# Kernel optimization log

Hardware: AMD Instinct MI355X
Metric: run time of the kernel (lower is better)

Reference implementation:

```python
import jax, jax.numpy as jnp
import numpy as np

H = 4            # num_heads
D_HID = 128      # n_hidden (per head)
IN = 256         # in_feats
C = 47           # n_classes
NEG = 0.2        # DGL GATConv default negative_slope
NUM_SRC = (150000, 25000, 6000)
NUM_DST = (25000, 6000, 1024)
NUM_EDGES = (375000, 90000, 10240)


def gat_conv(h_src, h_dst, src, dst, Wsrc, Wdst, al, ar, b, num_dst, out_dim, apply_act):
    # h_src: [Ns, Fin], h_dst: [Nd, Fin]; Wsrc/Wdst: [H*out, Fin]; al/ar: [H, out]; b: [H*out]
    fs = (h_src @ Wsrc.T).reshape(-1, H, out_dim)          # [Ns,H,out]
    fd = (h_dst @ Wdst.T).reshape(-1, H, out_dim)          # [Nd,H,out]
    el = jnp.einsum('nhd,hd->nh', fs, al)                  # [Ns,H]
    er = jnp.einsum('nhd,hd->nh', fd, ar)                  # [Nd,H]
    e = jax.nn.leaky_relu(el[src] + er[dst], NEG)          # [E,H]
    # numerically-stable edge softmax per dst node
    m = jax.ops.segment_max(e, dst, num_segments=num_dst)  # [Nd,H]
    m = jnp.where(jnp.isfinite(m), m, 0.0)                 # guard isolated dst nodes
    ex = jnp.exp(e - m[dst])                               # [E,H]
    s = jax.ops.segment_sum(ex, dst, num_segments=num_dst) # [Nd,H]
    # weighted neighbor aggregation (scatter-add), normalize after the sum
    agg = jax.ops.segment_sum(ex[:, :, None] * fs[src], dst, num_segments=num_dst)  # [Nd,H,out]
    rst = agg / jnp.maximum(s, 1e-9)[:, :, None]
    rst = rst + b.reshape(1, H, out_dim)
    if apply_act:
        rst = jax.nn.elu(rst)
    return rst


def setup_inputs() -> dict:
    key = jax.random.key(0)
    ks = jax.random.split(key, 32)
    inp = {}
    inp['x'] = jax.random.normal(ks[0], (NUM_SRC[0], IN), dtype=jnp.float32)
    # sampled blocks as edge lists (dst nodes are prefix of src nodes)
    inp['src0'] = jax.random.randint(ks[1], (NUM_EDGES[0],), 0, NUM_SRC[0])
    inp['dst0'] = jax.random.randint(ks[2], (NUM_EDGES[0],), 0, NUM_DST[0])
    inp['src1'] = jax.random.randint(ks[3], (NUM_EDGES[1],), 0, NUM_SRC[1])
    inp['dst1'] = jax.random.randint(ks[4], (NUM_EDGES[1],), 0, NUM_DST[1])
    inp['src2'] = jax.random.randint(ks[5], (NUM_EDGES[2],), 0, NUM_SRC[2])
    inp['dst2'] = jax.random.randint(ks[6], (NUM_EDGES[2],), 0, NUM_DST[2])
    # layer params: (in_dim, out_per_head): (256,128), (512,128), (512,47)
    dims = [(IN, D_HID), (H * D_HID, D_HID), (H * D_HID, C)]
    k = 7
    for l, (fin, fout) in enumerate(dims):
        inp[f'Wsrc{l}'] = jax.random.normal(ks[k], (H * fout, fin), dtype=jnp.float32) * 0.05; k += 1
        inp[f'Wdst{l}'] = jax.random.normal(ks[k], (H * fout, fin), dtype=jnp.float32) * 0.05; k += 1
        inp[f'al{l}'] = jax.random.normal(ks[k], (H, fout), dtype=jnp.float32) * 0.05; k += 1
        inp[f'ar{l}'] = jax.random.normal(ks[k], (H, fout), dtype=jnp.float32) * 0.05; k += 1
        inp[f'b{l}'] = jnp.zeros((H * fout,), dtype=jnp.float32); k += 1
    return inp


def reference(x, src0, dst0, src1, dst1, src2, dst2,
              Wsrc0, Wdst0, al0, ar0, b0,
              Wsrc1, Wdst1, al1, ar1, b1,
              Wsrc2, Wdst2, al2, ar2, b2):
    h = x
    # layer 0
    h = gat_conv(h, h[:NUM_DST[0]], src0, dst0, Wsrc0, Wdst0, al0, ar0, b0,
                 NUM_DST[0], D_HID, True).reshape(NUM_DST[0], H * D_HID)
    # layer 1
    h = gat_conv(h, h[:NUM_DST[1]], src1, dst1, Wsrc1, Wdst1, al1, ar1, b1,
                 NUM_DST[1], D_HID, True).reshape(NUM_DST[1], H * D_HID)
    # layer 2 (no activation), mean over heads, log-softmax
    h = gat_conv(h, h[:NUM_DST[2]], src2, dst2, Wsrc2, Wdst2, al2, ar2, b2,
                 NUM_DST[2], C, False)                      # [1024,H,C]
    h = h.mean(axis=1)                                      # [1024,C]
    return jax.nn.log_softmax(h, axis=-1)
```

## Files before the change

### kernel.cpp

```cpp
#include <hip/hip_runtime.h>
#include <math.h>


#define E0 375000
#define E1 90000
#define E2 10240
#define ETOT (E0 + E1 + E2)
#define ND0 25000
#define ND1 6000
#define ND2 1024
#define NTOT (ND0 + ND1 + ND2)
#define NCH ((NTOT + 127) / 128)

static const int L_NS[3]   = {150000, 25000, 6000};
static const int L_ND[3]   = {ND0, ND1, ND2};
static const int L_FIN[3]  = {256, 512, 512};
static const int L_FOUT[3] = {128, 128, 47};

typedef short bf8_t __attribute__((ext_vector_type(8)));
typedef float f32x4 __attribute__((ext_vector_type(4)));

__device__ __forceinline__ float lrelu(float v) { return v >= 0.f ? v : 0.2f * v; }
__device__ __forceinline__ unsigned short f2b(float f) {
  unsigned u = __float_as_uint(f);
  unsigned r = u + 0x7fffu + ((u >> 16) & 1u);
  return (unsigned short)(r >> 16);
}
__device__ __forceinline__ float b2f(unsigned v) {
  return __uint_as_float(v << 16);
}

__device__ __forceinline__ void gload16(const unsigned short* g, unsigned short* l) {
  __builtin_amdgcn_global_load_lds(
      (const __attribute__((address_space(1))) unsigned int*)g,
      (__attribute__((address_space(3))) unsigned int*)l, 16, 0, 0);
}


__global__ void k_prep_count(
    const int* __restrict__ d0, const int* __restrict__ d1,
    const int* __restrict__ d2, int* __restrict__ cntAll, int* __restrict__ r,
    const float* __restrict__ Ws0, const float* __restrict__ Wd0,
    const float* __restrict__ al0, const float* __restrict__ ar0,
    const float* __restrict__ Ws1, const float* __restrict__ Wd1,
    const float* __restrict__ al1, const float* __restrict__ ar1,
    const float* __restrict__ Ws2, const float* __restrict__ Wd2,
    const float* __restrict__ al2, const float* __restrict__ ar2,
    unsigned short* __restrict__ wlrb, float* __restrict__ wlr1,
    float* __restrict__ wlr2,
    unsigned short* __restrict__ B0, unsigned short* __restrict__ B1,
    unsigned short* __restrict__ B2) {
  int gid = blockIdx.x * 256 + threadIdx.x;
  if (gid < ETOT) {
    int goff, dv;
    if (gid < E0) { goff = 0; dv = d0[gid]; }
    else if (gid < E0 + E1) { goff = ND0; dv = d1[gid - E0]; }
    else { goff = ND0 + ND1; dv = d2[gid - E0 - E1]; }
    r[gid] = atomicAdd(&cntAll[goff + dv], 1);
  }
  if (gid < 2048) {
    int h = gid >> 8, k = gid & 255;
    const float* W = (h < 4) ? Ws0 : Wd0;
    const float* a = (h < 4) ? al0 : ar0;
    int hh = h & 3;
    float acc = 0.f;
    for (int d = 0; d < 128; ++d)
      acc += a[hh * 128 + d] * W[(size_t)(hh * 128 + d) * 256 + k];
    wlrb[h * 264 + k] = f2b(acc);
  } else if (gid < 4096) {
    int idx = gid - 2048;
    wlrb[(8 + (idx >> 8)) * 264 + (idx & 255)] = 0;
  } else if (gid < 12288) {
    int idx = gid - 4096;
    float* wlr; const float *Ws, *Wd, *al, *ar; int Fout;
    if (idx < 4096) { wlr = wlr1; Ws = Ws1; Wd = Wd1; al = al1; ar = ar1; Fout = 128; }
    else { idx -= 4096; wlr = wlr2; Ws = Ws2; Wd = Wd2; al = al2; ar = ar2; Fout = 47; }
    int which = idx >> 11;
    int rem = idx & 2047;
    int h = rem >> 9, k = rem & 511;
    const float* W = which ? Wd : Ws;
    const float* a = which ? ar : al;
    float acc = 0.f;
    for (int d = 0; d < Fout; ++d)
      acc += a[h * Fout + d] * W[(size_t)(h * Fout + d) * 512 + k];
    wlr[which * 2048 + rem] = acc;
  }
  const int n0 = 512 * 256, n1 = 512 * 512, n2 = 188 * 512;
  for (int i = gid; i < n0 + n1 + n2; i += gridDim.x * 256) {
    if (i < n0) B0[i] = f2b(Ws0[i]);
    else if (i < n0 + n1) B1[i - n0] = f2b(Ws1[i - n0]);
    else B2[i - n0 - n1] = f2b(Ws2[i - n0 - n1]);
  }
}

__global__ __launch_bounds__(128) void k_scanA(const int* __restrict__ cnt,
                                               int* __restrict__ S,
                                               int* __restrict__ btot, int n) {
  __shared__ int wt[2];
  int c = blockIdx.x, t = threadIdx.x, lane = t & 63, w = t >> 6;
  int g = c * 128 + t;
  int v = (g < n) ? cnt[g] : 0;
  int incl = v;
  for (int off = 1; off < 64; off <<= 1) {
    int u = __shfl_up(incl, off);
    if (lane >= off) incl += u;
  }
  if (lane == 63) wt[w] = incl;
  __syncthreads();
  int base = (w == 1) ? wt[0] : 0;
  if (g < n) S[g] = incl - v + base;
  if (t == 127) btot[c] = wt[0] + wt[1];
}

__global__ __launch_bounds__(256) void k_scanB(const int* __restrict__ btot,
                                               int* __restrict__ S, int n, int etot) {
  __shared__ int tv[256];
  int c = blockIdx.x, t = threadIdx.x;
  int own = (t < NCH) ? btot[t] : 0;
  tv[t] = own;
  __syncthreads();
  for (int off = 1; off < 256; off <<= 1) {
    int u = (t >= off) ? tv[t - off] : 0;
    __syncthreads();
    tv[t] += u;
    __syncthreads();
  }
  int base = tv[c] - btot[c];
  int g = c * 128 + (t & 127);
  if (t < 128 && g < n) S[g] += base;
  if (c == 0 && t == 255) S[n] = etot;
}

__global__ void k_scatter_all(
    const int* __restrict__ s0, const int* __restrict__ d0,
    const int* __restrict__ s1, const int* __restrict__ d1,
    const int* __restrict__ s2, const int* __restrict__ d2,
    const int* __restrict__ S, const int* __restrict__ r,
    int* __restrict__ cvAll) {
  int g = blockIdx.x * 256 + threadIdx.x;
  if (g >= ETOT) return;
  int goff, dv, sv;
  if (g < E0) { goff = 0; dv = d0[g]; sv = s0[g]; }
  else if (g < E0 + E1) { int e = g - E0; goff = ND0; dv = d1[e]; sv = s1[e]; }
  else { int e = g - E0 - E1; goff = ND0 + ND1; dv = d2[e]; sv = s2[e]; }
  cvAll[S[goff + dv] + r[g]] = sv;
}


__global__ __launch_bounds__(256) void k_dotc_mfma(
    const float* __restrict__ x, const unsigned short* __restrict__ wlrb,
    float* __restrict__ ell, float* __restrict__ err, int Ns, int Nd) {
  __shared__ unsigned short As[128 * 72];
  __shared__ unsigned short Bs[16 * 264];
  const int tid = threadIdx.x;
  const int w = tid >> 6, lane = tid & 63;
  const int bm = blockIdx.x * 128;
  const int rowg = tid >> 4;
  const int seg  = tid & 15;
  for (int i = tid; i < 16 * 264; i += 256) Bs[i] = wlrb[i];
  f32x4 acc[2] = {};
  for (int k0 = 0; k0 < 256; k0 += 64) {
    __syncthreads();
#pragma unroll
    for (int i = 0; i < 8; ++i) {
      int row = rowg + i * 16;
      int gm = bm + row;
      int gmc = gm < Ns ? gm : Ns - 1;
      float4 a = *reinterpret_cast<const float4*>(x + (size_t)gmc * 256 + k0 + seg * 4);
      ushort4 ub;
      ub.x = f2b(a.x); ub.y = f2b(a.y); ub.z = f2b(a.z); ub.w = f2b(a.w);
      *reinterpret_cast<ushort4*>(&As[row * 72 + seg * 4]) = ub;
    }
    __syncthreads();
    const int ra = w * 32 + (lane & 15);
    const int kf = (lane >> 4) * 8;
#pragma unroll
    for (int ks = 0; ks < 2; ++ks) {
      bf8_t b0 = *reinterpret_cast<const bf8_t*>(&Bs[(lane & 15) * 264 + k0 + ks * 32 + kf]);
      bf8_t a0 = *reinterpret_cast<const bf8_t*>(&As[ra * 72 + ks * 32 + kf]);
      bf8_t a1 = *reinterpret_cast<const bf8_t*>(&As[(ra + 16) * 72 + ks * 32 + kf]);
      acc[0] = __builtin_amdgcn_mfma_f32_16x16x32_bf16(a0, b0, acc[0], 0, 0, 0);
      acc[1] = __builtin_amdgcn_mfma_f32_16x16x32_bf16(a1, b0, acc[1], 0, 0, 0);
    }
  }
  int col = lane & 15;
#pragma unroll
  for (int fm = 0; fm < 2; ++fm) {
#pragma unroll
    for (int j = 0; j < 4; ++j) {
      int node = bm + w * 32 + fm * 16 + (lane >> 4) * 4 + j;
      if (node >= Ns) continue;
      float v = acc[fm][j];
      if (col < 4) ell[(size_t)node * 4 + col] = v;
      else if (col < 8 && node < Nd) err[(size_t)node * 4 + (col - 4)] = v;
    }
  }
}

__device__ __forceinline__ void reduce8_store(float v[8], int lane, int node, int Nd,
                                              float* __restrict__ ell,
                                              float* __restrict__ err) {
#pragma unroll
  for (int h = 0; h < 8; ++h) {
    v[h] += __shfl_xor(v[h], 8);
    v[h] += __shfl_xor(v[h], 16);
    v[h] += __shfl_xor(v[h], 32);
  }
  int sel = lane >> 3;
  float t01 = (sel & 1) ? v[1] : v[0];
  float t23 = (sel & 1) ? v[3] : v[2];
  float t45 = (sel & 1) ? v[5] : v[4];
  float t67 = (sel & 1) ? v[7] : v[6];
  float t03 = (sel & 2) ? t23 : t01;
  float t47 = (sel & 2) ? t67 : t45;
  float s   = (sel & 4) ? t47 : t03;
  s += __shfl_xor(s, 1);
  s += __shfl_xor(s, 2);
  s += __shfl_xor(s, 4);
  if ((lane & 7) == 0) {
    if (sel < 4) ell[(size_t)node * 4 + sel] = s;
    else if (node < Nd) err[(size_t)node * 4 + (sel - 4)] = s;
  }
}

__global__ __launch_bounds__(256) void k_dot_bf(
    const unsigned short* __restrict__ Hs, const float* __restrict__ wlr,
    float* __restrict__ ell, float* __restrict__ err, int Ns, int Nd) {
  int node = blockIdx.x * 4 + (threadIdx.x >> 6);
  int lane = threadIdx.x & 63;
  if (node >= Ns) return;
  uint4 raw = *reinterpret_cast<const uint4*>(Hs + (size_t)node * 512 + lane * 8);
  float xv[8];
  xv[0] = b2f(raw.x & 0xffffu); xv[1] = b2f(raw.x >> 16);
  xv[2] = b2f(raw.y & 0xffffu); xv[3] = b2f(raw.y >> 16);
  xv[4] = b2f(raw.z & 0xffffu); xv[5] = b2f(raw.z >> 16);
  xv[6] = b2f(raw.w & 0xffffu); xv[7] = b2f(raw.w >> 16);
  bool nR = node < Nd;
  float v[8];
#pragma unroll
  for (int h = 0; h < 4; ++h) {
    const float* wp = wlr + h * 512 + lane * 8;
    float4 w0 = *reinterpret_cast<const float4*>(wp);
    float4 w1 = *reinterpret_cast<const float4*>(wp + 4);
    v[h] = xv[0]*w0.x + xv[1]*w0.y + xv[2]*w0.z + xv[3]*w0.w +
           xv[4]*w1.x + xv[5]*w1.y + xv[6]*w1.z + xv[7]*w1.w;
    v[4 + h] = 0.f;
    if (nR) {
      const float* wq = wlr + 2048 + h * 512 + lane * 8;
      float4 u0 = *reinterpret_cast<const float4*>(wq);
      float4 u1 = *reinterpret_cast<const float4*>(wq + 4);
      v[4 + h] = xv[0]*u0.x + xv[1]*u0.y + xv[2]*u0.z + xv[3]*u0.w +
                 xv[4]*u1.x + xv[5]*u1.y + xv[6]*u1.z + xv[7]*u1.w;
    }
  }
  reduce8_store(v, lane, node, Nd, ell, err);
}

#define GAT_ACCF(w4, xr)                                                       \
  {                                                                            \
    float w0 = w4.x, w1 = w4.y, w2 = w4.z, w3 = w4.w;                          \
    s0 += w0; s1 += w1; s2 += w2; s3 += w3;                                    \
    float x0 = xr.x, x1 = xr.y, x2 = xr.z, x3 = xr.w;                          \
    acc[0][0] = fmaf(w0, x0, acc[0][0]); acc[0][1] = fmaf(w0, x1, acc[0][1]);  \
    acc[0][2] = fmaf(w0, x2, acc[0][2]); acc[0][3] = fmaf(w0, x3, acc[0][3]);  \
    acc[1][0] = fmaf(w1, x0, acc[1][0]); acc[1][1] = fmaf(w1, x1, acc[1][1]);  \
    acc[1][2] = fmaf(w1, x2, acc[1][2]); acc[1][3] = fmaf(w1, x3, acc[1][3]);  \
    acc[2][0] = fmaf(w2, x0, acc[2][0]); acc[2][1] = fmaf(w2, x1, acc[2][1]);  \
    acc[2][2] = fmaf(w2, x2, acc[2][2]); acc[2][3] = fmaf(w2, x3, acc[2][3]);  \
    acc[3][0] = fmaf(w3, x0, acc[3][0]); acc[3][1] = fmaf(w3, x1, acc[3][1]);  \
    acc[3][2] = fmaf(w3, x2, acc[3][2]); acc[3][3] = fmaf(w3, x3, acc[3][3]);  \
  }

__global__ __launch_bounds__(256) void k_gather4_f32(
    const float* __restrict__ X, const float* __restrict__ ell,
    const float* __restrict__ err, const int* __restrict__ rowptr,
    const int* __restrict__ colv, unsigned short* __restrict__ Z, int Nd) {
  constexpr int CAP = 256;
  __shared__ float4 esm_all[4][CAP];
  __shared__ int csm_all[4][CAP];
  int w = threadIdx.x >> 6, lane = threadIdx.x & 63;
  int n = blockIdx.x * 4 + w;
  if (n >= Nd) return;
  float4* esm = esm_all[w];
  int* csm = csm_all[w];
  int beg = rowptr[n], cnt = rowptr[n + 1] - beg;
  float4 er4 = *reinterpret_cast<const float4*>(err + (size_t)n * 4);
  float m0 = -INFINITY, m1 = -INFINITY, m2 = -INFINITY, m3 = -INFINITY;
  for (int i = lane; i < cnt; i += 64) {
    int c = colv[beg + i];
    float4 el4 = *reinterpret_cast<const float4*>(ell + (size_t)c * 4);
    float4 e4;
    e4.x = lrelu(el4.x + er4.x); e4.y = lrelu(el4.y + er4.y);
    e4.z = lrelu(el4.z + er4.z); e4.w = lrelu(el4.w + er4.w);
    if (i < CAP) { csm[i] = c; esm[i] = e4; }
    m0 = fmaxf(m0, e4.x); m1 = fmaxf(m1, e4.y);
    m2 = fmaxf(m2, e4.z); m3 = fmaxf(m3, e4.w);
  }
  for (int off = 32; off > 0; off >>= 1) {
    m0 = fmaxf(m0, __shfl_xor(m0, off));
    m1 = fmaxf(m1, __shfl_xor(m1, off));
    m2 = fmaxf(m2, __shfl_xor(m2, off));
    m3 = fmaxf(m3, __shfl_xor(m3, off));
  }
  __builtin_amdgcn_sched_barrier(0);
  float s0 = 0.f, s1 = 0.f, s2 = 0.f, s3 = 0.f;
  float acc[4][4] = {};
  if (cnt <= CAP) {
    for (int i = lane; i < cnt; i += 64) {
      float4 e = esm[i];
      esm[i] = make_float4(__expf(e.x - m0), __expf(e.y - m1),
                           __expf(e.z - m2), __expf(e.w - m3));
    }
    __builtin_amdgcn_sched_barrier(0);
    int j = 0;
    for (; j + 4 <= cnt; j += 4) {
      int c0 = csm[j], c1 = csm[j + 1], c2 = csm[j + 2], c3 = csm[j + 3];
      float4 wa = esm[j], wb = esm[j + 1], wc = esm[j + 2], wd = esm[j + 3];
      float4 xa = *reinterpret_cast<const float4*>(X + (size_t)c0 * 256 + lane * 4);
      float4 xb = *reinterpret_cast<const float4*>(X + (size_t)c1 * 256 + lane * 4);
      float4 xc = *reinterpret_cast<const float4*>(X + (size_t)c2 * 256 + lane * 4);
      float4 xd = *reinterpret_cast<const float4*>(X + (size_t)c3 * 256 + lane * 4);
      GAT_ACCF(wa, xa); GAT_ACCF(wb, xb); GAT_ACCF(wc, xc); GAT_ACCF(wd, xd);
    }
    for (; j < cnt; ++j) {
      float4 wa = esm[j];
      float4 xa = *reinterpret_cast<const float4*>(X + (size_t)csm[j] * 256 + lane * 4);
      GAT_ACCF(wa, xa);
    }
  } else {
    for (int j = 0; j < cnt; ++j) {
      int c = colv[beg + j];
      float4 el4 = *reinterpret_cast<const float4*>(ell + (size_t)c * 4);
      float4 w4;
      w4.x = __expf(lrelu(el4.x + er4.x) - m0);
      w4.y = __expf(lrelu(el4.y + er4.y) - m1);
      w4.z = __expf(lrelu(el4.z + er4.z) - m2);
      w4.w = __expf(lrelu(el4.w + er4.w) - m3);
      float4 xa = *reinterpret_cast<const float4*>(X + (size_t)c * 256 + lane * 4);
      GAT_ACCF(w4, xa);
    }
  }
  float inv[4];
  inv[0] = 1.f / fmaxf(s0, 1e-9f); inv[1] = 1.f / fmaxf(s1, 1e-9f);
  inv[2] = 1.f / fmaxf(s2, 1e-9f); inv[3] = 1.f / fmaxf(s3, 1e-9f);
#pragma unroll
  for (int h = 0; h < 4; ++h) {
    ushort4 o;
    o.x = f2b(acc[h][0] * inv[h]); o.y = f2b(acc[h][1] * inv[h]);
    o.z = f2b(acc[h][2] * inv[h]); o.w = f2b(acc[h][3] * inv[h]);
    *reinterpret_cast<ushort4*>(Z + (size_t)n * 1024 + h * 256 + lane * 4) = o;
  }
}

#define GAT_ACC(w4, xr)                                                        \
  {                                                                            \
    float w0 = w4.x, w1 = w4.y, w2 = w4.z, w3 = w4.w;                          \
    s0 += w0; s1 += w1; s2 += w2; s3 += w3;                                    \
    float x0 = b2f(xr.x), x1 = b2f(xr.y), x2 = b2f(xr.z), x3 = b2f(xr.w);      \
    acc[0][0] = fmaf(w0, x0, acc[0][0]); acc[0][1] = fmaf(w0, x1, acc[0][1]);  \
    acc[0][2] = fmaf(w0, x2, acc[0][2]); acc[0][3] = fmaf(w0, x3, acc[0][3]);  \
    acc[1][0] = fmaf(w1, x0, acc[1][0]); acc[1][1] = fmaf(w1, x1, acc[1][1]);  \
    acc[1][2] = fmaf(w1, x2, acc[1][2]); acc[1][3] = fmaf(w1, x3, acc[1][3]);  \
    acc[2][0] = fmaf(w2, x0, acc[2][0]); acc[2][1] = fmaf(w2, x1, acc[2][1]);  \
    acc[2][2] = fmaf(w2, x2, acc[2][2]); acc[2][3] = fmaf(w2, x3, acc[2][3]);  \
    acc[3][0] = fmaf(w3, x0, acc[3][0]); acc[3][1] = fmaf(w3, x1, acc[3][1]);  \
    acc[3][2] = fmaf(w3, x2, acc[3][2]); acc[3][3] = fmaf(w3, x3, acc[3][3]);  \
  }

__global__ __launch_bounds__(128) void k_gather_512(
    const unsigned short* __restrict__ Hs, const float* __restrict__ ell,
    const float* __restrict__ err, const int* __restrict__ rowptr,
    const int* __restrict__ colv, unsigned short* __restrict__ Z) {
  constexpr int TB = 128;
  constexpr int CAP = 256;
  int n = blockIdx.x, t = threadIdx.x;
  int beg = rowptr[n], cnt = rowptr[n + 1] - beg;
  float4 er4 = *reinterpret_cast<const float4*>(err + (size_t)n * 4);
  __shared__ float4 esm[CAP];
  __shared__ int csm[CAP];
  __shared__ float4 wred[2];
  float m0 = -INFINITY, m1 = -INFINITY, m2 = -INFINITY, m3 = -INFINITY;
  for (int i = t; i < cnt; i += TB) {
    int c = colv[beg + i];
    float4 el4 = *reinterpret_cast<const float4*>(ell + (size_t)c * 4);
    float4 e4;
    e4.x = lrelu(el4.x + er4.x); e4.y = lrelu(el4.y + er4.y);
    e4.z = lrelu(el4.z + er4.z); e4.w = lrelu(el4.w + er4.w);
    if (i < CAP) { csm[i] = c; esm[i] = e4; }
    m0 = fmaxf(m0, e4.x); m1 = fmaxf(m1, e4.y);
    m2 = fmaxf(m2, e4.z); m3 = fmaxf(m3, e4.w);
  }
  for (int off = 32; off > 0; off >>= 1) {
    m0 = fmaxf(m0, __shfl_xor(m0, off));
    m1 = fmaxf(m1, __shfl_xor(m1, off));
    m2 = fmaxf(m2, __shfl_xor(m2, off));
    m3 = fmaxf(m3, __shfl_xor(m3, off));
  }
  if ((t & 63) == 0) wred[t >> 6] = make_float4(m0, m1, m2, m3);
  __syncthreads();
  {
    float4 wa = wred[0], wb = wred[1];
    m0 = fmaxf(wa.x, wb.x); m1 = fmaxf(wa.y, wb.y);
    m2 = fmaxf(wa.z, wb.z); m3 = fmaxf(wa.w, wb.w);
  }
  float s0 = 0.f, s1 = 0.f, s2 = 0.f, s3 = 0.f;
  float acc[4][4] = {};
  if (cnt <= CAP) {
    for (int i = t; i < cnt; i += TB) {
      float4 e = esm[i];
      esm[i] = make_float4(__expf(e.x - m0), __expf(e.y - m1),
                           __expf(e.z - m2), __expf(e.w - m3));
    }
    __syncthreads();
    int j = 0;
    for (; j + 2 <= cnt; j += 2) {
      float4 wa = esm[j], wb = esm[j + 1];
      int ca = csm[j], cb = csm[j + 1];
      ushort4 xa = *reinterpret_cast<const ushort4*>(Hs + (size_t)ca * 512 + t * 4);
      ushort4 xb = *reinterpret_cast<const ushort4*>(Hs + (size_t)cb * 512 + t * 4);
      GAT_ACC(wa, xa);
      GAT_ACC(wb, xb);
    }
    if (j < cnt) {
      float4 wa = esm[j];
      ushort4 xa = *reinterpret_cast<const ushort4*>(Hs + (size_t)csm[j] * 512 + t * 4);
      GAT_ACC(wa, xa);
    }
  } else {
    for (int j = 0; j < cnt; ++j) {
      int c = colv[beg + j];
      float4 el4 = *reinterpret_cast<const float4*>(ell + (size_t)c * 4);
      float4 w4;
      w4.x = __expf(lrelu(el4.x + er4.x) - m0);
      w4.y = __expf(lrelu(el4.y + er4.y) - m1);
      w4.z = __expf(lrelu(el4.z + er4.z) - m2);
      w4.w = __expf(lrelu(el4.w + er4.w) - m3);
      ushort4 xa = *reinterpret_cast<const ushort4*>(Hs + (size_t)c * 512 + t * 4);
      GAT_ACC(w4, xa);
    }
  }
  float inv[4];
  inv[0] = 1.f / fmaxf(s0, 1e-9f); inv[1] = 1.f / fmaxf(s1, 1e-9f);
  inv[2] = 1.f / fmaxf(s2, 1e-9f); inv[3] = 1.f / fmaxf(s3, 1e-9f);
#pragma unroll
  for (int h = 0; h < 4; ++h) {
    ushort4 o;
    o.x = f2b(acc[h][0] * inv[h]); o.y = f2b(acc[h][1] * inv[h]);
    o.z = f2b(acc[h][2] * inv[h]); o.w = f2b(acc[h][3] * inv[h]);
    *reinterpret_cast<ushort4*>(Z + (size_t)n * 2048 + h * 512 + t * 4) = o;
  }
}
#undef GAT_ACC
#undef GAT_ACCF

template <int BN, bool ACT, bool OUTBF>
__global__ __launch_bounds__(256) void k_gemm_mfma(
    const unsigned short* __restrict__ Zb, const unsigned short* __restrict__ Wb,
    const float* __restrict__ bias, void* __restrict__ outv,
    int M, int N, int K) {
  constexpr int FN = BN / 16;
  constexpr int AI = 4;
  constexpr int BI = BN / 32;
  int h = blockIdx.z;
  __shared__ unsigned short As[128 * 64];
  __shared__ unsigned short Bs[BN * 64];
  const int tid = threadIdx.x;
  const int w = tid >> 6, lane = tid & 63;
  const int bm = blockIdx.x * 128, bn = blockIdx.y * BN;
  const int lda = 4 * K;
  const unsigned short* Ag = Zb + (size_t)h * K;
  const unsigned short* Bg = Wb + (size_t)h * N * K;
  const int lrow = lane >> 3;
  const int gseg = (lane & 7) ^ lrow;
  f32x4 acc[2][FN];
#pragma unroll
  for (int i = 0; i < 2; ++i)
#pragma unroll
    for (int j = 0; j < FN; ++j) acc[i][j] = (f32x4){0.f, 0.f, 0.f, 0.f};

  for (int k0 = 0; k0 < K; k0 += 64) {
    __syncthreads();
#pragma unroll
    for (int i = 0; i < AI; ++i) {
      int ch = w * AI + i;
      int row = ch * 8 + lrow;
      int gm = bm + row; gm = gm < M ? gm : M - 1;
      gload16(Ag + (size_t)gm * lda + k0 + gseg * 8, As + ch * 512);
    }
#pragma unroll
    for (int i = 0; i < BI; ++i) {
      int ch = w * BI + i;
      int row = ch * 8 + lrow;
      int gn = bn + row; gn = gn < N ? gn : N - 1;
      gload16(Bg + (size_t)gn * K + k0 + gseg * 8, Bs + ch * 512);
    }
    __syncthreads();
    const int ra = w * 32 + (lane & 15);
#pragma unroll
    for (int ks = 0; ks < 2; ++ks) {
      int cs = ((((ks << 2) + (lane >> 4)) ^ (lane & 7)) << 3);
      bf8_t a0 = *reinterpret_cast<const bf8_t*>(As + ra * 64 + cs);
      bf8_t a1 = *reinterpret_cast<const bf8_t*>(As + (ra + 16) * 64 + cs);
#pragma unroll
      for (int fn = 0; fn < FN; ++fn) {
        bf8_t bf = *reinterpret_cast<const bf8_t*>(Bs + (fn * 16 + (lane & 15)) * 64 + cs);
        acc[0][fn] = __builtin_amdgcn_mfma_f32_16x16x32_bf16(a0, bf, acc[0][fn], 0, 0, 0);
        acc[1][fn] = __builtin_amdgcn_mfma_f32_16x16x32_bf16(a1, bf, acc[1][fn], 0, 0, 0);
      }
    }
  }
  int ldo = 4 * N;
#pragma unroll
  for (int fm = 0; fm < 2; ++fm) {
#pragma unroll
    for (int fn = 0; fn < FN; ++fn) {
      int colb = bn + fn * 16 + (lane & 15);
      if (colb >= N) continue;
      float bv = bias[h * N + colb];
#pragma unroll
      for (int j = 0; j < 4; ++j) {
        int rowb = bm + w * 32 + fm * 16 + (lane >> 4) * 4 + j;
        if (rowb >= M) continue;
        float v = acc[fm][fn][j] + bv;
        if (ACT) v = v > 0.f ? v : (__expf(v) - 1.f);
        size_t off = (size_t)rowb * ldo + (size_t)h * N + colb;
        if (OUTBF) ((unsigned short*)outv)[off] = f2b(v);
        else ((float*)outv)[off] = v;
      }
    }
  }
}

__global__ __launch_bounds__(256) void k_mean_lsm(const float* __restrict__ rst2,
                                                  float* __restrict__ out, int Nd) {
  int node = blockIdx.x * 4 + (threadIdx.x >> 6);
  int lane = threadIdx.x & 63;
  if (node >= Nd) return;
  const float* r = rst2 + (size_t)node * 188;
  float vv = 0.f;
  if (lane < 47)
    vv = 0.25f * (r[lane] + r[47 + lane] + r[94 + lane] + r[141 + lane]);
  float m = (lane < 47) ? vv : -INFINITY;
  for (int off = 32; off > 0; off >>= 1) m = fmaxf(m, __shfl_xor(m, off));
  float ex = (lane < 47) ? __expf(vv - m) : 0.f;
  float ss = ex;
  for (int off = 32; off > 0; off >>= 1) ss += __shfl_xor(ss, off);
  if (lane < 47) out[(size_t)node * 47 + lane] = vv - m - logf(ss);
}

extern "C" void kernel_launch(void* const* d_in, const int* in_sizes, int n_in,
                              void* d_out, int out_size, void* d_ws, size_t ws_size,
                              hipStream_t stream) {
  (void)in_sizes; (void)n_in; (void)out_size; (void)ws_size;
  const float* x = (const float*)d_in[0];
  const int* srcs[3] = {(const int*)d_in[1], (const int*)d_in[3], (const int*)d_in[5]};
  const int* dsts[3] = {(const int*)d_in[2], (const int*)d_in[4], (const int*)d_in[6]};
  const float* Wsrc[3] = {(const float*)d_in[7], (const float*)d_in[12], (const float*)d_in[17]};
  const float* Wdst[3] = {(const float*)d_in[8], (const float*)d_in[13], (const float*)d_in[18]};
  const float* al[3]   = {(const float*)d_in[9], (const float*)d_in[14], (const float*)d_in[19]};
  const float* ar[3]   = {(const float*)d_in[10], (const float*)d_in[15], (const float*)d_in[20]};
  const float* bb[3]   = {(const float*)d_in[11], (const float*)d_in[16], (const float*)d_in[21]};

  char* p = (char*)d_ws;
  auto alloc = [&](size_t bytes) -> void* {
    void* r = (void*)p;
    p += (bytes + 255) & ~(size_t)255;
    return r;
  };
  unsigned short* zbf = (unsigned short*)alloc((size_t)25000 * 1024 * 2);
  unsigned short* h1  = (unsigned short*)alloc((size_t)25000 * 512 * 2);
  unsigned short* h2  = (unsigned short*)alloc((size_t)6000 * 512 * 2);
  float* rst2   = (float*)alloc((size_t)1024 * 188 * 4);
  unsigned short* Wb0 = (unsigned short*)alloc((size_t)512 * 256 * 2);
  unsigned short* Wb1 = (unsigned short*)alloc((size_t)512 * 512 * 2);
  unsigned short* Wb2 = (unsigned short*)alloc((size_t)188 * 512 * 2);
  float* ell    = (float*)alloc((size_t)150000 * 4 * 4);
  float* err    = (float*)alloc((size_t)25000 * 4 * 4);
  int* cntAll   = (int*)alloc((size_t)NTOT * 4);
  int* Sarr     = (int*)alloc((size_t)(NTOT + 8) * 4);
  int* btot     = (int*)alloc((size_t)((NCH + 7) & ~7) * 4);
  int* r_all    = (int*)alloc((size_t)ETOT * 4);
  int* cvAll    = (int*)alloc((size_t)ETOT * 4);
  unsigned short* wlrb = (unsigned short*)alloc((size_t)16 * 264 * 2);
  float* wlr1   = (float*)alloc((size_t)8 * 512 * 4);
  float* wlr2   = (float*)alloc((size_t)8 * 512 * 4);

  hipMemsetAsync(cntAll, 0, (size_t)NTOT * 4, stream);
  k_prep_count<<<(ETOT + 255) / 256, 256, 0, stream>>>(
      dsts[0], dsts[1], dsts[2], cntAll, r_all,
      Wsrc[0], Wdst[0], al[0], ar[0], Wsrc[1], Wdst[1], al[1], ar[1],
      Wsrc[2], Wdst[2], al[2], ar[2], wlrb, wlr1, wlr2, Wb0, Wb1, Wb2);
  k_scanA<<<NCH, 128, 0, stream>>>(cntAll, Sarr, btot, NTOT);
  k_scanB<<<NCH, 256, 0, stream>>>(btot, Sarr, NTOT, ETOT);
  k_scatter_all<<<(ETOT + 255) / 256, 256, 0, stream>>>(
      srcs[0], dsts[0], srcs[1], dsts[1], srcs[2], dsts[2], Sarr, r_all, cvAll);

  const unsigned short* Hbf[3] = {nullptr, h1, h2};
  const unsigned short* Wbf[3] = {Wb0, Wb1, Wb2};
  const float* wlrs[3] = {nullptr, wlr1, wlr2};
  const int noff[3] = {0, ND0, ND0 + ND1};

  for (int l = 0; l < 3; ++l) {
    int Ns = L_NS[l], Nd = L_ND[l], Fin = L_FIN[l], Fout = L_FOUT[l];
    if (l == 0) {
      k_dotc_mfma<<<(Ns + 127) / 128, 256, 0, stream>>>(x, wlrb, ell, err, Ns, Nd);
      k_gather4_f32<<<(Nd + 3) / 4, 256, 0, stream>>>(
          x, ell, err, Sarr + noff[l], cvAll, zbf, Nd);
    } else {
      k_dot_bf<<<(Ns + 3) / 4, 256, 0, stream>>>(Hbf[l], wlrs[l], ell, err, Ns, Nd);
      k_gather_512<<<Nd, 128, 0, stream>>>(
          Hbf[l], ell, err, Sarr + noff[l], cvAll, zbf);
    }
    dim3 g((Nd + 127) / 128, 1, 4);
    if (l == 0)
      k_gemm_mfma<128, true, true><<<g, 256, 0, stream>>>(zbf, Wbf[l], bb[l], h1, Nd, Fout, Fin);
    else if (l == 1)
      k_gemm_mfma<128, true, true><<<g, 256, 0, stream>>>(zbf, Wbf[l], bb[l], h2, Nd, Fout, Fin);
    else
      k_gemm_mfma<64, false, false><<<g, 256, 0, stream>>>(zbf, Wbf[l], bb[l], rst2, Nd, Fout, Fin);
  }
  k_mean_lsm<<<(1024 + 3) / 4, 256, 0, stream>>>(rst2, (float*)d_out, 1024);
}
```

Baseline: 289.0 us.

## Use MFMA GEMM for attention logits and atomic cursor CSR scatter

Layers 1 and 2 previously computed the per-node attention logits with a per-wavefront dot-product kernel and shuffle reductions. They now use a bf16 MFMA tile kernel against bf16-packed folded attention weights, and the fp32 folded-weight buffers become bf16. The CSR build also stops recording per-edge ranks during counting and instead uses an atomic cursor per destination during scatter, which removes the rank array. Neighbour order inside each destination segment becomes nondeterministic, and the logit weights carry bf16 rounding.

Result: slower. 295.7 us (+2.3%).

```diff
diff --git a/kernel.cpp b/kernel.cpp
--- a/kernel.cpp
+++ b/kernel.cpp
@@ -39,15 +39,15 @@
 
 __global__ void k_prep_count(
     const int* __restrict__ d0, const int* __restrict__ d1,
-    const int* __restrict__ d2, int* __restrict__ cntAll, int* __restrict__ r,
+    const int* __restrict__ d2, int* __restrict__ cntAll,
     const float* __restrict__ Ws0, const float* __restrict__ Wd0,
     const float* __restrict__ al0, const float* __restrict__ ar0,
     const float* __restrict__ Ws1, const float* __restrict__ Wd1,
     const float* __restrict__ al1, const float* __restrict__ ar1,
     const float* __restrict__ Ws2, const float* __restrict__ Wd2,
     const float* __restrict__ al2, const float* __restrict__ ar2,
-    unsigned short* __restrict__ wlrb, float* __restrict__ wlr1,
-    float* __restrict__ wlr2,
+    unsigned short* __restrict__ wlrb, unsigned short* __restrict__ wblr1,
+    unsigned short* __restrict__ wblr2,
     unsigned short* __restrict__ B0, unsigned short* __restrict__ B1,
     unsigned short* __restrict__ B2) {
   int gid = blockIdx.x * 256 + threadIdx.x;
@@ -56,7 +56,7 @@
     if (gid < E0) { goff = 0; dv = d0[gid]; }
     else if (gid < E0 + E1) { goff = ND0; dv = d1[gid - E0]; }
     else { goff = ND0 + ND1; dv = d2[gid - E0 - E1]; }
-    r[gid] = atomicAdd(&cntAll[goff + dv], 1);
+    atomicAdd(&cntAll[goff + dv], 1);
   }
   if (gid < 2048) {
     int h = gid >> 8, k = gid & 255;
@@ -72,18 +72,17 @@
     wlrb[(8 + (idx >> 8)) * 264 + (idx & 255)] = 0;
   } else if (gid < 12288) {
     int idx = gid - 4096;
-    float* wlr; const float *Ws, *Wd, *al, *ar; int Fout;
-    if (idx < 4096) { wlr = wlr1; Ws = Ws1; Wd = Wd1; al = al1; ar = ar1; Fout = 128; }
-    else { idx -= 4096; wlr = wlr2; Ws = Ws2; Wd = Wd2; al = al2; ar = ar2; Fout = 47; }
-    int which = idx >> 11;
-    int rem = idx & 2047;
-    int h = rem >> 9, k = rem & 511;
-    const float* W = which ? Wd : Ws;
-    const float* a = which ? ar : al;
+    unsigned short* wb; const float *Ws, *Wd, *al, *ar; int Fout;
+    if (idx < 4096) { wb = wblr1; Ws = Ws1; Wd = Wd1; al = al1; ar = ar1; Fout = 128; }
+    else { idx -= 4096; wb = wblr2; Ws = Ws2; Wd = Wd2; al = al2; ar = ar2; Fout = 47; }
+    int r = idx >> 9, k = idx & 511;
+    const float* W = (r < 4) ? Ws : Wd;
+    const float* a = (r < 4) ? al : ar;
+    int hh = r & 3;
     float acc = 0.f;
     for (int d = 0; d < Fout; ++d)
-      acc += a[h * Fout + d] * W[(size_t)(h * Fout + d) * 512 + k];
-    wlr[which * 2048 + rem] = acc;
+      acc += a[hh * Fout + d] * W[(size_t)(hh * Fout + d) * 512 + k];
+    wb[r * 512 + k] = f2b(acc);
   }
   const int n0 = 512 * 256, n1 = 512 * 512, n2 = 188 * 512;
   for (int i = gid; i < n0 + n1 + n2; i += gridDim.x * 256) {
@@ -113,7 +112,9 @@
 }
 
 __global__ __launch_bounds__(256) void k_scanB(const int* __restrict__ btot,
-                                               int* __restrict__ S, int n, int etot) {
+                                               int* __restrict__ S,
+                                               int* __restrict__ cursor,
+                                               int n, int etot) {
   __shared__ int tv[256];
   int c = blockIdx.x, t = threadIdx.x;
   int own = (t < NCH) ? btot[t] : 0;
@@ -127,7 +128,11 @@
   }
   int base = tv[c] - btot[c];
   int g = c * 128 + (t & 127);
-  if (t < 128 && g < n) S[g] += base;
+  if (t < 128 && g < n) {
+    int s = S[g] + base;
+    S[g] = s;
+    cursor[g] = s;
+  }
   if (c == 0 && t == 255) S[n] = etot;
 }
 
@@ -135,15 +140,15 @@
     const int* __restrict__ s0, const int* __restrict__ d0,
     const int* __restrict__ s1, const int* __restrict__ d1,
     const int* __restrict__ s2, const int* __restrict__ d2,
-    const int* __restrict__ S, const int* __restrict__ r,
-    int* __restrict__ cvAll) {
+    int* __restrict__ cursor, int* __restrict__ cvAll) {
   int g = blockIdx.x * 256 + threadIdx.x;
   if (g >= ETOT) return;
   int goff, dv, sv;
   if (g < E0) { goff = 0; dv = d0[g]; sv = s0[g]; }
   else if (g < E0 + E1) { int e = g - E0; goff = ND0; dv = d1[e]; sv = s1[e]; }
   else { int e = g - E0 - E1; goff = ND0 + ND1; dv = d2[e]; sv = s2[e]; }
-  cvAll[S[goff + dv] + r[g]] = sv;
+  int slot = atomicAdd(&cursor[goff + dv], 1);
+  cvAll[slot] = sv;
 }
 
 
@@ -197,63 +202,65 @@
   }
 }
 
-__device__ __forceinline__ void reduce8_store(float v[8], int lane, int node, int Nd,
-                                              float* __restrict__ ell,
-                                              float* __restrict__ err) {
-#pragma unroll
-  for (int h = 0; h < 8; ++h) {
-    v[h] += __shfl_xor(v[h], 8);
-    v[h] += __shfl_xor(v[h], 16);
-    v[h] += __shfl_xor(v[h], 32);
-  }
-  int sel = lane >> 3;
-  float t01 = (sel & 1) ? v[1] : v[0];
-  float t23 = (sel & 1) ? v[3] : v[2];
-  float t45 = (sel & 1) ? v[5] : v[4];
-  float t67 = (sel & 1) ? v[7] : v[6];
-  float t03 = (sel & 2) ? t23 : t01;
-  float t47 = (sel & 2) ? t67 : t45;
-  float s   = (sel & 4) ? t47 : t03;
-  s += __shfl_xor(s, 1);
-  s += __shfl_xor(s, 2);
-  s += __shfl_xor(s, 4);
-  if ((lane & 7) == 0) {
-    if (sel < 4) ell[(size_t)node * 4 + sel] = s;
-    else if (node < Nd) err[(size_t)node * 4 + (sel - 4)] = s;
-  }
-}
-
-__global__ __launch_bounds__(256) void k_dot_bf(
-    const unsigned short* __restrict__ Hs, const float* __restrict__ wlr,
-    float* __restrict__ ell, float* __restrict__ err, int Ns, int Nd) {
-  int node = blockIdx.x * 4 + (threadIdx.x >> 6);
-  int lane = threadIdx.x & 63;
-  if (node >= Ns) return;
-  uint4 raw = *reinterpret_cast<const uint4*>(Hs + (size_t)node * 512 + lane * 8);
-  float xv[8];
-  xv[0] = b2f(raw.x & 0xffffu); xv[1] = b2f(raw.x >> 16);
-  xv[2] = b2f(raw.y & 0xffffu); xv[3] = b2f(raw.y >> 16);
-  xv[4] = b2f(raw.z & 0xffffu); xv[5] = b2f(raw.z >> 16);
-  xv[6] = b2f(raw.w & 0xffffu); xv[7] = b2f(raw.w >> 16);
-  bool nR = node < Nd;
-  float v[8];
-#pragma unroll
-  for (int h = 0; h < 4; ++h) {
-    const float* wp = wlr + h * 512 + lane * 8;
-    float4 w0 = *reinterpret_cast<const float4*>(wp);
-    float4 w1 = *reinterpret_cast<const float4*>(wp + 4);
-    v[h] = xv[0]*w0.x + xv[1]*w0.y + xv[2]*w0.z + xv[3]*w0.w +
-           xv[4]*w1.x + xv[5]*w1.y + xv[6]*w1.z + xv[7]*w1.w;
-    v[4 + h] = 0.f;
-    if (nR) {
-      const float* wq = wlr + 2048 + h * 512 + lane * 8;
-      float4 u0 = *reinterpret_cast<const float4*>(wq);
-      float4 u1 = *reinterpret_cast<const float4*>(wq + 4);
-      v[4 + h] = xv[0]*u0.x + xv[1]*u0.y + xv[2]*u0.z + xv[3]*u0.w +
-                 xv[4]*u1.x + xv[5]*u1.y + xv[6]*u1.z + xv[7]*u1.w;
-    }
-  }
-  reduce8_store(v, lane, node, Nd, ell, err);
+__global__ __launch_bounds__(256) void k_dot_gemm(
+    const unsigned short* __restrict__ Hs, const unsigned short* __restrict__ Wb8,
+    float* __restrict__ ell, float* __restrict__ err, int M, int Nd) {
+  constexpr int K = 512;
+  __shared__ unsigned short As[128 * 64];
+  __shared__ unsigned short Bs[32 * 64];
+  const int tid = threadIdx.x;
+  const int w = tid >> 6, lane = tid & 63;
+  const int bm = blockIdx.x * 128;
+  const int lrow = lane >> 3;
+  const int gseg = (lane & 7) ^ lrow;
+  f32x4 acc[2][2];
+#pragma unroll
+  for (int i = 0; i < 2; ++i)
+#pragma unroll
+    for (int j = 0; j < 2; ++j) acc[i][j] = (f32x4){0.f, 0.f, 0.f, 0.f};
+
+  for (int k0 = 0; k0 < K; k0 += 64) {
+    __syncthreads();
+#pragma unroll
+    for (int i = 0; i < 4; ++i) {
+      int ch = w * 4 + i;
+      int row = ch * 8 + lrow;
+      int gm = bm + row; gm = gm < M ? gm : M - 1;
+      gload16(Hs + (size_t)gm * K + k0 + gseg * 8, As + ch * 512);
+    }
+    {
+      int ch = w;
+      int row = ch * 8 + lrow;
+      int gn = row < 8 ? row : 7;
+      gload16(Wb8 + (size_t)gn * K + k0 + gseg * 8, Bs + ch * 512);
+    }
+    __syncthreads();
+    const int ra = w * 32 + (lane & 15);
+#pragma unroll
+    for (int ks = 0; ks < 2; ++ks) {
+      int cs = ((((ks << 2) + (lane >> 4)) ^ (lane & 7)) << 3);
+      bf8_t a0 = *reinterpret_cast<const bf8_t*>(As + ra * 64 + cs);
+      bf8_t a1 = *reinterpret_cast<const bf8_t*>(As + (ra + 16) * 64 + cs);
+#pragma unroll
+      for (int fn = 0; fn < 2; ++fn) {
+        bf8_t bf = *reinterpret_cast<const bf8_t*>(Bs + (fn * 16 + (lane & 15)) * 64 + cs);
+        acc[0][fn] = __builtin_amdgcn_mfma_f32_16x16x32_bf16(a0, bf, acc[0][fn], 0, 0, 0);
+        acc[1][fn] = __builtin_amdgcn_mfma_f32_16x16x32_bf16(a1, bf, acc[1][fn], 0, 0, 0);
+      }
+    }
+  }
+  int col = lane & 15;
+#pragma unroll
+  for (int fm = 0; fm < 2; ++fm) {
+#pragma unroll
+    for (int j = 0; j < 4; ++j) {
+      int node = bm + w * 32 + fm * 16 + (lane >> 4) * 4 + j;
+      if (node >= M) continue;
+      float v = acc[fm][0][j];
+      if (col < 4) ell[(size_t)node * 4 + col] = v;
+      else if (col < 8 && node < Nd) err[(size_t)node * 4 + (col - 4)] = v;
+    }
+  }
 }
 
 #define GAT_ACCF(w4, xr)                                                       \
@@ -578,26 +585,26 @@
   float* err    = (float*)alloc((size_t)25000 * 4 * 4);
   int* cntAll   = (int*)alloc((size_t)NTOT * 4);
   int* Sarr     = (int*)alloc((size_t)(NTOT + 8) * 4);
+  int* cursor   = (int*)alloc((size_t)NTOT * 4);
   int* btot     = (int*)alloc((size_t)((NCH + 7) & ~7) * 4);
-  int* r_all    = (int*)alloc((size_t)ETOT * 4);
   int* cvAll    = (int*)alloc((size_t)ETOT * 4);
-  unsigned short* wlrb = (unsigned short*)alloc((size_t)16 * 264 * 2);
-  float* wlr1   = (float*)alloc((size_t)8 * 512 * 4);
-  float* wlr2   = (float*)alloc((size_t)8 * 512 * 4);
+  unsigned short* wlrb  = (unsigned short*)alloc((size_t)16 * 264 * 2);
+  unsigned short* wblr1 = (unsigned short*)alloc((size_t)8 * 512 * 2);
+  unsigned short* wblr2 = (unsigned short*)alloc((size_t)8 * 512 * 2);
 
   hipMemsetAsync(cntAll, 0, (size_t)NTOT * 4, stream);
   k_prep_count<<<(ETOT + 255) / 256, 256, 0, stream>>>(
-      dsts[0], dsts[1], dsts[2], cntAll, r_all,
+      dsts[0], dsts[1], dsts[2], cntAll,
       Wsrc[0], Wdst[0], al[0], ar[0], Wsrc[1], Wdst[1], al[1], ar[1],
-      Wsrc[2], Wdst[2], al[2], ar[2], wlrb, wlr1, wlr2, Wb0, Wb1, Wb2);
+      Wsrc[2], Wdst[2], al[2], ar[2], wlrb, wblr1, wblr2, Wb0, Wb1, Wb2);
   k_scanA<<<NCH, 128, 0, stream>>>(cntAll, Sarr, btot, NTOT);
-  k_scanB<<<NCH, 256, 0, stream>>>(btot, Sarr, NTOT, ETOT);
+  k_scanB<<<NCH, 256, 0, stream>>>(btot, Sarr, cursor, NTOT, ETOT);
   k_scatter_all<<<(ETOT + 255) / 256, 256, 0, stream>>>(
-      srcs[0], dsts[0], srcs[1], dsts[1], srcs[2], dsts[2], Sarr, r_all, cvAll);
+      srcs[0], dsts[0], srcs[1], dsts[1], srcs[2], dsts[2], cursor, cvAll);
 
   const unsigned short* Hbf[3] = {nullptr, h1, h2};
   const unsigned short* Wbf[3] = {Wb0, Wb1, Wb2};
-  const float* wlrs[3] = {nullptr, wlr1, wlr2};
+  const unsigned short* wblr[3] = {nullptr, wblr1, wblr2};
   const int noff[3] = {0, ND0, ND0 + ND1};
 
   for (int l = 0; l < 3; ++l) {
@@ -607,7 +614,8 @@
       k_gather4_f32<<<(Nd + 3) / 4, 256, 0, stream>>>(
           x, ell, err, Sarr + noff[l], cvAll, zbf, Nd);
     } else {
-      k_dot_bf<<<(Ns + 3) / 4, 256, 0, stream>>>(Hbf[l], wlrs[l], ell, err, Ns, Nd);
+      k_dot_gemm<<<(Ns + 127) / 128, 256, 0, stream>>>(
+          Hbf[l], wblr[l], ell, err, Ns, Nd);
       k_gather_512<<<Nd, 128, 0, stream>>>(
           Hbf[l], ell, err, Sarr + noff[l], cvAll, zbf);
     }
```
